# Optimization experiments

Measured on AMD Instinct MI355X. Metric: run time of the kernel, lower is better.

## Reference

```python
import jax, jax.numpy as jnp
import numpy as np

E = 11      # num_experts
K = 6       # active_experts
P = 64      # prototype_dim
NH = 4      # attention heads
HD = P // NH


def setup_inputs() -> dict:
    key = jax.random.key(0)
    ks = jax.random.split(key, 24)
    B, C, H, W = 8, 128, 64, 64
    hid = 4 * C
    s = lambda k, shape, sc=0.02: jax.random.normal(k, shape, dtype=jnp.float32) * sc
    # orthogonal-ish prototypes via QR
    q, _ = jnp.linalg.qr(jax.random.normal(ks[1], (P, P), dtype=jnp.float32))
    return {
        "x": jax.random.normal(ks[0], (B, C, H, W), dtype=jnp.float32),
        "proto": q[:E, :],                       # (E, P)
        "ctx_w": s(ks[2], (P, C)), "ctx_b": jnp.zeros((P,), jnp.float32),
        "inp_w": s(ks[3], (P, C)), "inp_b": jnp.zeros((P,), jnp.float32),
        "wq": s(ks[4], (P, P)), "bq": jnp.zeros((P,), jnp.float32),
        "wk": s(ks[5], (P, P)), "bk": jnp.zeros((P,), jnp.float32),
        "wv": s(ks[6], (P, P)), "bv": jnp.zeros((P,), jnp.float32),
        "wo": s(ks[7], (P, P)), "bo": jnp.zeros((P,), jnp.float32),
        "ln_g": jnp.ones((P,), jnp.float32), "ln_b": jnp.zeros((P,), jnp.float32),
        "ew1": s(ks[8], (E, hid, C)), "eb1": jnp.zeros((E, hid), jnp.float32),
        "ew2": s(ks[9], (E, C, hid)), "eb2": jnp.zeros((E, C), jnp.float32),
    }


def _layernorm(x, g, b, eps=1e-5):
    m = x.mean(-1, keepdims=True)
    v = ((x - m) ** 2).mean(-1, keepdims=True)
    return (x - m) * jax.lax.rsqrt(v + eps) * g + b


def _forward(x, proto, ctx_w, ctx_b, inp_w, inp_b,
             wq, bq, wk, bk, wv, bv, wo, bo, ln_g, ln_b,
             ew1, eb1, ew2, eb2):
    B, C, H, W = x.shape
    # --- router: global context + prototype interaction ---
    gc = jnp.einsum("bchw->bc", x) / (H * W)          # (B, C) mean over HW
    gc = gc @ ctx_w.T + ctx_b                          # (B, P)
    seq = jnp.concatenate([gc[:, None, :],
                           jnp.broadcast_to(proto[None], (B, E, P))], axis=1)  # (B, E+1, P)
    S = E + 1
    q = (seq @ wq.T + bq).reshape(B, S, NH, HD)
    k = (seq @ wk.T + bk).reshape(B, S, NH, HD)
    v = (seq @ wv.T + bv).reshape(B, S, NH, HD)
    att = jax.nn.softmax(jnp.einsum("bqhd,bkhd->bhqk", q, k) / jnp.sqrt(jnp.float32(HD)), axis=-1)
    ao = jnp.einsum("bhqk,bkhd->bqhd", att, v).reshape(B, S, P) @ wo.T + bo
    seq2 = _layernorm(ao + seq, ln_g, ln_b)
    up = seq2[:, 1:, :]                                # (B, E, P) updated prototypes
    # --- per-pixel routing logits ---
    xr = jnp.einsum("bchw,pc->bphw", x, inp_w) + inp_b[None, :, None, None]
    logits = jnp.einsum("bphw,bep->behw", xr, up) / jnp.sqrt(jnp.float32(P))
    probs = jax.nn.softmax(logits, axis=1)             # (B, E, H, W)
    pt = probs.transpose(0, 2, 3, 1)                   # (B, H, W, E)
    tv, ti = jax.lax.top_k(pt, K)                      # (B, H, W, K)
    tv = tv / tv.sum(-1, keepdims=True)
    oh = jax.nn.one_hot(ti, E, dtype=x.dtype)          # (B, H, W, K, E)
    mask = (oh * tv[..., None]).sum(-2)                # (B, H, W, E) scatter of routing weights
    # --- dense expert loop with per-pixel masking ---
    final = jnp.zeros_like(x)
    for e in range(E):
        h = jax.nn.gelu(jnp.einsum("bchw,oc->bohw", x, ew1[e]) + eb1[e][None, :, None, None],
                        approximate=False)
        y = jnp.einsum("bohw,co->bchw", h, ew2[e]) + eb2[e][None, :, None, None]
        final = final + mask[..., e][:, None, :, :] * y
    # --- aux losses ---
    mean_prob = probs.mean((0, 2, 3))                  # (E,)
    mean_load = oh.sum(-2).mean((0, 1, 2))             # (E,)
    aux = E * jnp.sum(mean_prob * mean_load)
    pn = proto / jnp.linalg.norm(proto, axis=1, keepdims=True)
    corr = pn @ pn.T
    ortho = jnp.linalg.norm(corr - jnp.eye(E, dtype=x.dtype))
    return x + final, aux + 0.5 * ortho


def reference(x, proto, ctx_w, ctx_b, inp_w, inp_b,
              wq, bq, wk, bk, wv, bv, wo, bo, ln_g, ln_b,
              ew1, eb1, ew2, eb2):
    return _forward(x, proto, ctx_w, ctx_b, inp_w, inp_b,
                    wq, bq, wk, bk, wv, bv, wo, bo, ln_g, ln_b,
                    ew1, eb1, ew2, eb2)
```

## Files before the change

kernel.cpp:

```cpp
#include <hip/hip_runtime.h>

#define NE 11
#define NP 64
#define NC 128
#define NHW 4096
#define NHID 512
#define NB 8

typedef __attribute__((ext_vector_type(8))) __bf16 bf16x8;
typedef __attribute__((ext_vector_type(4))) float f32x4;

__device__ __forceinline__ unsigned short f2bf(float f) {
    unsigned u = __float_as_uint(f);
    unsigned r = (u + 0x7fffu + ((u >> 16) & 1u)) >> 16;
    return (unsigned short)r;
}

__device__ __forceinline__ float gelu_f(float v) {
    return 0.5f * v * (1.0f + erff(v * 0.70710678118654752440f));
}

__device__ __forceinline__ bf16x8 ldsB(const unsigned short* basep, int row, int col) {
    int byteoff = ((row << 8) + (col << 1)) ^ ((row & 7) << 4);
    return *(const bf16x8*)((const char*)basep + byteoff);
}

__global__ void k_cvt(const float* __restrict__ ew1, const float* __restrict__ ew2,
                      unsigned short* __restrict__ o1, unsigned short* __restrict__ o2) {
    const int n = NE * NHID * NC;
    for (int i = blockIdx.x * 256 + threadIdx.x; i < n; i += gridDim.x * 256) {
        o1[i] = f2bf(ew1[i]);
        o2[i] = f2bf(ew2[i]);
    }
}

__global__ void k_gc(const float* __restrict__ x, float* __restrict__ gc) {
    int row = blockIdx.x;
    const float* p = x + (size_t)row * NHW;
    float s = 0.f;
    for (int i = threadIdx.x; i < NHW; i += 256) s += p[i];
    __shared__ float red[256];
    red[threadIdx.x] = s;
    __syncthreads();
    for (int off = 128; off > 0; off >>= 1) {
        if (threadIdx.x < off) red[threadIdx.x] += red[threadIdx.x + off];
        __syncthreads();
    }
    if (threadIdx.x == 0) gc[row] = red[0] * (1.0f / 4096.0f);
}

__global__ void k_attn(const float* __restrict__ gc, const float* __restrict__ proto,
                       const float* __restrict__ ctx_w, const float* __restrict__ ctx_b,
                       const float* __restrict__ wq, const float* __restrict__ bq,
                       const float* __restrict__ wk, const float* __restrict__ bk,
                       const float* __restrict__ wv, const float* __restrict__ bv,
                       const float* __restrict__ wo, const float* __restrict__ bo,
                       const float* __restrict__ lng, const float* __restrict__ lnb,
                       float* __restrict__ up, float* __restrict__ ortho, float* __restrict__ stats) {
    int t = threadIdx.x;
    __shared__ float seq[12][64], qs[12][64], ks_[12][64], vs[12][64], ao[12][64], rr[12][64];
    __shared__ float nr[NE], sq[NE * NE];

    if (blockIdx.x == 8) {
        if (t < 22) stats[t] = 0.0f;
        if (t < NE) {
            float s = 0.f;
            for (int p = 0; p < NP; p++) { float v = proto[t * NP + p]; s += v * v; }
            nr[t] = rsqrtf(s);
        }
        __syncthreads();
        if (t < NE * NE) {
            int i = t / NE, j = t % NE;
            float d = 0.f;
            for (int p = 0; p < NP; p++) d += proto[i * NP + p] * proto[j * NP + p];
            float c = d * nr[i] * nr[j] - (i == j ? 1.0f : 0.0f);
            sq[t] = c * c;
        }
        __syncthreads();
        if (t == 0) {
            float s = 0.f;
            for (int i = 0; i < NE * NE; i++) s += sq[i];
            *ortho = sqrtf(s);
        }
        return;
    }

    int b = blockIdx.x;
    if (t < NP) {
        float a = ctx_b[t];
        for (int c = 0; c < NC; c++) a = fmaf(gc[b * NC + c], ctx_w[t * NC + c], a);
        seq[0][t] = a;
    }
    for (int i = t; i < NE * NP; i += 256) { int e = i >> 6, p = i & 63; seq[e + 1][p] = proto[e * NP + p]; }
    __syncthreads();
    for (int i = t; i < 12 * NP; i += 256) {
        int s = i >> 6, p = i & 63;
        float aq = bq[p], ak = bk[p], av = bv[p];
        for (int pp = 0; pp < NP; pp++) {
            float sv = seq[s][pp];
            aq = fmaf(sv, wq[p * NP + pp], aq);
            ak = fmaf(sv, wk[p * NP + pp], ak);
            av = fmaf(sv, wv[p * NP + pp], av);
        }
        qs[s][p] = aq; ks_[s][p] = ak; vs[s][p] = av;
    }
    __syncthreads();
    if (t < 48) {
        int h = t / 12, qq = t % 12;
        float sc[12], m = -1e30f;
        for (int kk = 0; kk < 12; kk++) {
            float s = 0.f;
            for (int d = 0; d < 16; d++) s = fmaf(qs[qq][h * 16 + d], ks_[kk][h * 16 + d], s);
            s *= 0.25f;
            sc[kk] = s;
            if (s > m) m = s;
        }
        float den = 0.f;
        for (int kk = 0; kk < 12; kk++) { sc[kk] = expf(sc[kk] - m); den += sc[kk]; }
        float inv = 1.0f / den;
        for (int d = 0; d < 16; d++) {
            float a = 0.f;
            for (int kk = 0; kk < 12; kk++) a = fmaf(sc[kk], vs[kk][h * 16 + d], a);
            ao[qq][h * 16 + d] = a * inv;
        }
    }
    __syncthreads();
    for (int i = t; i < 12 * NP; i += 256) {
        int s = i >> 6, p = i & 63;
        float a = bo[p];
        for (int pp = 0; pp < NP; pp++) a = fmaf(ao[s][pp], wo[p * NP + pp], a);
        rr[s][p] = a + seq[s][p];
    }
    __syncthreads();
    if (t < 12) {
        int s = t;
        float m = 0.f;
        for (int p = 0; p < NP; p++) m += rr[s][p];
        m *= (1.0f / 64.0f);
        float v = 0.f;
        for (int p = 0; p < NP; p++) { float d = rr[s][p] - m; v += d * d; }
        v *= (1.0f / 64.0f);
        float is = rsqrtf(v + 1e-5f);
        if (s >= 1)
            for (int p = 0; p < NP; p++)
                up[(b * NE + s - 1) * NP + p] = (rr[s][p] - m) * is * lng[p] + lnb[p];
    }
}

__global__ __launch_bounds__(256, 2) void k_main(
    const float* __restrict__ x, const float* __restrict__ inp_w, const float* __restrict__ inp_b,
    const unsigned short* __restrict__ ew1b, const float* __restrict__ eb1,
    const unsigned short* __restrict__ ew2b, const float* __restrict__ eb2,
    const float* __restrict__ upw, float* __restrict__ stats, float* __restrict__ out) {
    int tid = threadIdx.x;
    int bimg = blockIdx.x >> 6;
    int pix0 = (blockIdx.x & 63) << 6;
    int wid = tid >> 6;
    int l15 = tid & 15;
    int l4 = (tid >> 4) & 3;

    __shared__ __align__(16) unsigned short xs[64 * 128];
    __shared__ __align__(16) unsigned short hs[64 * 128];
    __shared__ float stage[32 * 64];
    __shared__ float lpart[4][NE][64];
    __shared__ float upl[NE * NP];
    __shared__ float wm[NE * 64];
    __shared__ float pb[NE * 64];
    __shared__ unsigned smask[64];
    __shared__ float eb1c[128], eb2l[128];
    __shared__ int eflag[NE];

    for (int i = tid; i < NE * NP; i += 256) upl[i] = upw[bimg * (NE * NP) + i];
    int pixl = tid & 63;
    int pg = wid;
    float xr[16];
#pragma unroll
    for (int p = 0; p < 16; p++) xr[p] = inp_b[pg * 16 + p];

    for (int cb = 0; cb < NC; cb += 32) {
        for (int i = tid; i < 32 * 64; i += 256) {
            int cc = i >> 6, px = i & 63;
            float v = x[(size_t)(bimg * NC + cb + cc) * NHW + pix0 + px];
            stage[cc * 64 + px] = v;
            int byteoff = ((px << 8) + ((cb + cc) << 1)) ^ ((px & 7) << 4);
            *(unsigned short*)((char*)xs + byteoff) = f2bf(v);
        }
        __syncthreads();
#pragma unroll 4
        for (int cc = 0; cc < 32; cc++) {
            float xv = stage[cc * 64 + pixl];
#pragma unroll
            for (int p = 0; p < 16; p++)
                xr[p] = fmaf(inp_w[(pg * 16 + p) * NC + cb + cc], xv, xr[p]);
        }
        __syncthreads();
    }
    for (int e = 0; e < NE; e++) {
        float a = 0.f;
#pragma unroll
        for (int p = 0; p < 16; p++) a = fmaf(upl[e * NP + pg * 16 + p], xr[p], a);
        lpart[pg][e][pixl] = a;
    }
    __syncthreads();

    if (tid < 64) {
        float pr[NE];
        float mx = -1e30f;
        for (int e = 0; e < NE; e++) {
            float l = (lpart[0][e][tid] + lpart[1][e][tid] + lpart[2][e][tid] + lpart[3][e][tid]) * 0.125f;
            pr[e] = l;
            if (l > mx) mx = l;
        }
        float den = 0.f;
        for (int e = 0; e < NE; e++) { pr[e] = expf(pr[e] - mx); den += pr[e]; }
        float inv = 1.0f / den;
        for (int e = 0; e < NE; e++) { pr[e] *= inv; pb[e * 64 + tid] = pr[e]; }
        unsigned used = 0;
        float tvsum = 0.f;
        float wloc[NE];
        for (int e = 0; e < NE; e++) wloc[e] = 0.f;
        for (int k = 0; k < 6; k++) {
            int best = 0;
            float bv = -1.0f;
            for (int e = 0; e < NE; e++)
                if (!((used >> e) & 1) && pr[e] > bv) { bv = pr[e]; best = e; }
            used |= 1u << best;
            wloc[best] = bv;
            tvsum += bv;
        }
        float itv = 1.0f / tvsum;
        for (int e = 0; e < NE; e++) wm[e * 64 + tid] = wloc[e] * itv;
        smask[tid] = used;
    }
    __syncthreads();
    if (tid < NE) {
        float sp = 0.f;
        int cnt = 0;
        for (int px = 0; px < 64; px++) {
            sp += pb[tid * 64 + px];
            cnt += (smask[px] >> tid) & 1;
        }
        atomicAdd(&stats[tid], sp);
        atomicAdd(&stats[NE + tid], (float)cnt);
        eflag[tid] = cnt;
    }
    __syncthreads();

    float outacc[2][4][4];
    for (int ct = 0; ct < 2; ct++)
        for (int nt = 0; nt < 4; nt++)
            for (int r = 0; r < 4; r++) outacc[ct][nt][r] = 0.f;

    for (int e = 0; e < NE; e++) {
        if (eflag[e] == 0) continue;
        __syncthreads();
        if (tid < 128) eb2l[tid] = eb2[e * NC + tid];
        f32x4 acc2[2][4];
        for (int ct = 0; ct < 2; ct++)
            for (int nt = 0; nt < 4; nt++)
                for (int r = 0; r < 4; r++) acc2[ct][nt][r] = 0.f;

        for (int j = 0; j < 4; j++) {
            if (tid < 128) eb1c[tid] = eb1[e * NHID + j * 128 + tid];
            bf16x8 a1[2][4];
#pragma unroll
            for (int ot = 0; ot < 2; ot++)
#pragma unroll
                for (int ksp = 0; ksp < 4; ksp++) {
                    const unsigned short* src =
                        ew1b + (size_t)(e * NHID + j * 128 + (wid * 2 + ot) * 16 + l15) * NC + ksp * 32 + l4 * 8;
                    a1[ot][ksp] = *(const bf16x8*)src;
                }
            f32x4 acc1[2][4];
            for (int ot = 0; ot < 2; ot++)
                for (int nt = 0; nt < 4; nt++)
                    for (int r = 0; r < 4; r++) acc1[ot][nt][r] = 0.f;
#pragma unroll
            for (int nt = 0; nt < 4; nt++) {
#pragma unroll
                for (int ksp = 0; ksp < 4; ksp++) {
                    bf16x8 bf = ldsB(xs, nt * 16 + l15, ksp * 32 + l4 * 8);
                    acc1[0][nt] = __builtin_amdgcn_mfma_f32_16x16x32_bf16(a1[0][ksp], bf, acc1[0][nt], 0, 0, 0);
                    acc1[1][nt] = __builtin_amdgcn_mfma_f32_16x16x32_bf16(a1[1][ksp], bf, acc1[1][nt], 0, 0, 0);
                }
            }
            __syncthreads();
#pragma unroll
            for (int ot = 0; ot < 2; ot++)
                for (int nt = 0; nt < 4; nt++) {
                    int oloc = (wid * 2 + ot) * 16 + l4 * 4;
                    int px = nt * 16 + l15;
                    unsigned short h4[4];
#pragma unroll
                    for (int r = 0; r < 4; r++) {
                        float v = acc1[ot][nt][r] + eb1c[oloc + r];
                        h4[r] = f2bf(gelu_f(v));
                    }
                    unsigned lo = (unsigned)h4[0] | ((unsigned)h4[1] << 16);
                    unsigned hi = (unsigned)h4[2] | ((unsigned)h4[3] << 16);
                    int byteoff = ((px << 8) + (oloc << 1)) ^ ((px & 7) << 4);
                    *(uint2*)((char*)hs + byteoff) = make_uint2(lo, hi);
                }
            __syncthreads();
            bf16x8 a2[2][4];
#pragma unroll
            for (int ct = 0; ct < 2; ct++)
#pragma unroll
                for (int ksp = 0; ksp < 4; ksp++) {
                    const unsigned short* src =
                        ew2b + (size_t)(e * NC + (wid * 2 + ct) * 16 + l15) * NHID + j * 128 + ksp * 32 + l4 * 8;
                    a2[ct][ksp] = *(const bf16x8*)src;
                }
#pragma unroll
            for (int nt = 0; nt < 4; nt++) {
#pragma unroll
                for (int ksp = 0; ksp < 4; ksp++) {
                    bf16x8 bf = ldsB(hs, nt * 16 + l15, ksp * 32 + l4 * 8);
                    acc2[0][nt] = __builtin_amdgcn_mfma_f32_16x16x32_bf16(a2[0][ksp], bf, acc2[0][nt], 0, 0, 0);
                    acc2[1][nt] = __builtin_amdgcn_mfma_f32_16x16x32_bf16(a2[1][ksp], bf, acc2[1][nt], 0, 0, 0);
                }
            }
        }
#pragma unroll
        for (int ct = 0; ct < 2; ct++)
            for (int nt = 0; nt < 4; nt++) {
                int px = nt * 16 + l15;
                float w = wm[e * 64 + px];
                int cg = (wid * 2 + ct) * 16 + l4 * 4;
#pragma unroll
                for (int r = 0; r < 4; r++)
                    outacc[ct][nt][r] = fmaf(w, acc2[ct][nt][r] + eb2l[cg + r], outacc[ct][nt][r]);
            }
    }

#pragma unroll
    for (int ct = 0; ct < 2; ct++)
        for (int nt = 0; nt < 4; nt++) {
            int px = pix0 + nt * 16 + l15;
#pragma unroll
            for (int r = 0; r < 4; r++) {
                int c = (wid * 2 + ct) * 16 + l4 * 4 + r;
                size_t g = (size_t)(bimg * NC + c) * NHW + px;
                out[g] = x[g] + outacc[ct][nt][r];
            }
        }
}

__global__ void k_final(const float* __restrict__ stats, const float* __restrict__ ortho,
                        float* __restrict__ out) {
    if (threadIdx.x == 0 && blockIdx.x == 0) {
        float aux = 0.f;
        for (int e = 0; e < NE; e++)
            aux += (stats[e] * (1.0f / 32768.0f)) * (stats[NE + e] * (1.0f / 32768.0f));
        aux *= (float)NE;
        out[4194304] = aux + 0.5f * (*ortho);
    }
}

extern "C" void kernel_launch(void* const* d_in, const int* in_sizes, int n_in,
                              void* d_out, int out_size, void* d_ws, size_t ws_size,
                              hipStream_t stream) {
    const float* x = (const float*)d_in[0];
    const float* proto = (const float*)d_in[1];
    const float* ctx_w = (const float*)d_in[2];
    const float* ctx_b = (const float*)d_in[3];
    const float* inp_w = (const float*)d_in[4];
    const float* inp_b = (const float*)d_in[5];
    const float* wq = (const float*)d_in[6];
    const float* bq = (const float*)d_in[7];
    const float* wk = (const float*)d_in[8];
    const float* bk = (const float*)d_in[9];
    const float* wv = (const float*)d_in[10];
    const float* bv = (const float*)d_in[11];
    const float* wo = (const float*)d_in[12];
    const float* bo = (const float*)d_in[13];
    const float* lng = (const float*)d_in[14];
    const float* lnb = (const float*)d_in[15];
    const float* ew1 = (const float*)d_in[16];
    const float* eb1 = (const float*)d_in[17];
    const float* ew2 = (const float*)d_in[18];
    const float* eb2 = (const float*)d_in[19];
    float* out = (float*)d_out;
    float* ws = (float*)d_ws;

    float* gc = ws;
    float* up = ws + 1024;
    float* ortho = ws + 6656;
    float* stats = ws + 6657;
    unsigned short* ew1b = (unsigned short*)(ws + 8192);
    unsigned short* ew2b = ew1b + NE * NHID * NC;

    k_cvt<<<512, 256, 0, stream>>>(ew1, ew2, ew1b, ew2b);
    k_gc<<<1024, 256, 0, stream>>>(x, gc);
    k_attn<<<9, 256, 0, stream>>>(gc, proto, ctx_w, ctx_b, wq, bq, wk, bk, wv, bv, wo, bo, lng, lnb,
                                  up, ortho, stats);
    k_main<<<512, 256, 0, stream>>>(x, inp_w, inp_b, ew1b, eb1, ew2b, eb2, up, stats, out);
    k_final<<<1, 64, 0, stream>>>(stats, ortho, out);
}
```

Before: 432.3 us.

## Restructure expert MLP kernel with 8 waves, double-buffered hidden tile, fast GELU

Raises the main kernel to 512 threads, with each wave owning one 16-row tile instead of two, and double-buffers the hidden-activation LDS tile so each step needs one barrier instead of two. The routing weight is folded into the GELU output before the second GEMM, which removes the per-expert accumulator epilogue. Expert bias is added once at the end. It also replaces erff with a polynomial erf approximation built on hardware exp2/rcp, and computes stats with wave shuffles and ballots. The weight-conversion and mean kernels are merged into one launch. It drops the skip for experts no pixel in the tile uses, and the polynomial GELU adds small numerical error.

```diff
diff --git a/kernel.cpp b/kernel.cpp
--- a/kernel.cpp
+++ b/kernel.cpp
@@ -5,48 +5,67 @@
 #define NC 128
 #define NHW 4096
 #define NHID 512
-#define NB 8
 
 typedef __attribute__((ext_vector_type(8))) __bf16 bf16x8;
+typedef __attribute__((ext_vector_type(4))) __bf16 bf16x4;
 typedef __attribute__((ext_vector_type(4))) float f32x4;
 
+#if __has_builtin(__builtin_amdgcn_exp2f)
+#define FEXP2(x) __builtin_amdgcn_exp2f(x)
+#else
+#define FEXP2(x) exp2f(x)
+#endif
+#if __has_builtin(__builtin_amdgcn_rcpf)
+#define FRCP(x) __builtin_amdgcn_rcpf(x)
+#else
+#define FRCP(x) (1.0f / (x))
+#endif
+
 __device__ __forceinline__ unsigned short f2bf(float f) {
-    unsigned u = __float_as_uint(f);
-    unsigned r = (u + 0x7fffu + ((u >> 16) & 1u)) >> 16;
-    return (unsigned short)r;
-}
-
-__device__ __forceinline__ float gelu_f(float v) {
-    return 0.5f * v * (1.0f + erff(v * 0.70710678118654752440f));
-}
-
-__device__ __forceinline__ bf16x8 ldsB(const unsigned short* basep, int row, int col) {
-    int byteoff = ((row << 8) + (col << 1)) ^ ((row & 7) << 4);
-    return *(const bf16x8*)((const char*)basep + byteoff);
-}
-
-__global__ void k_cvt(const float* __restrict__ ew1, const float* __restrict__ ew2,
-                      unsigned short* __restrict__ o1, unsigned short* __restrict__ o2) {
-    const int n = NE * NHID * NC;
-    for (int i = blockIdx.x * 256 + threadIdx.x; i < n; i += gridDim.x * 256) {
-        o1[i] = f2bf(ew1[i]);
-        o2[i] = f2bf(ew2[i]);
-    }
-}
-
-__global__ void k_gc(const float* __restrict__ x, float* __restrict__ gc) {
-    int row = blockIdx.x;
-    const float* p = x + (size_t)row * NHW;
-    float s = 0.f;
-    for (int i = threadIdx.x; i < NHW; i += 256) s += p[i];
-    __shared__ float red[256];
-    red[threadIdx.x] = s;
-    __syncthreads();
-    for (int off = 128; off > 0; off >>= 1) {
-        if (threadIdx.x < off) red[threadIdx.x] += red[threadIdx.x + off];
-        __syncthreads();
-    }
-    if (threadIdx.x == 0) gc[row] = red[0] * (1.0f / 4096.0f);
+    return __builtin_bit_cast(unsigned short, (__bf16)f);
+}
+
+__device__ __forceinline__ float gelu_erf(float v) {
+    float av = fabsf(v);
+    float z = av * 0.70710678118654752440f;
+    float t = FRCP(fmaf(z, 0.3275911f, 1.0f));
+    float p = t * fmaf(t, fmaf(t, fmaf(t, fmaf(t, 1.061405429f, -1.453152027f),
+                                       1.421413741f), -0.284496736f), 0.254829592f);
+    float e = FEXP2(z * z * -1.44269504088896f);
+    float erfz = fmaf(-p, e, 1.0f);
+    float hv = 0.5f * av;
+    float g = fmaf(hv, erfz, hv);
+    return g + fminf(v, 0.0f);
+}
+
+__device__ __forceinline__ bf16x8 ldsB(const char* base, int row, int col) {
+    int off = ((row << 8) + (col << 1)) ^ ((row & 7) << 4);
+    return *(const bf16x8*)(base + off);
+}
+
+__global__ void k_prep(const float* __restrict__ ew1, const float* __restrict__ ew2,
+                       unsigned short* __restrict__ o1, unsigned short* __restrict__ o2,
+                       const float* __restrict__ x, float* __restrict__ gc) {
+    if (blockIdx.x < 512) {
+        const int n = NE * NHID * NC;
+        for (int i = blockIdx.x * 256 + threadIdx.x; i < n; i += 512 * 256) {
+            o1[i] = f2bf(ew1[i]);
+            o2[i] = f2bf(ew2[i]);
+        }
+    } else {
+        int row = blockIdx.x - 512;
+        const float* p = x + (size_t)row * NHW;
+        float s = 0.f;
+        for (int i = threadIdx.x; i < NHW; i += 256) s += p[i];
+        __shared__ float red[256];
+        red[threadIdx.x] = s;
+        __syncthreads();
+        for (int off = 128; off > 0; off >>= 1) {
+            if (threadIdx.x < off) red[threadIdx.x] += red[threadIdx.x + off];
+            __syncthreads();
+        }
+        if (threadIdx.x == 0) gc[row] = red[0] * (1.0f / 4096.0f);
+    }
 }
 
 __global__ void k_attn(const float* __restrict__ gc, const float* __restrict__ proto,
@@ -147,7 +166,7 @@
     }
 }
 
-__global__ __launch_bounds__(256, 2) void k_main(
+__global__ __launch_bounds__(512, 4) void k_main(
     const float* __restrict__ x, const float* __restrict__ inp_w, const float* __restrict__ inp_b,
     const unsigned short* __restrict__ ew1b, const float* __restrict__ eb1,
     const unsigned short* __restrict__ ew2b, const float* __restrict__ eb2,
@@ -159,191 +178,170 @@
     int l15 = tid & 15;
     int l4 = (tid >> 4) & 3;
 
-    __shared__ __align__(16) unsigned short xs[64 * 128];
-    __shared__ __align__(16) unsigned short hs[64 * 128];
-    __shared__ float stage[32 * 64];
-    __shared__ float lpart[4][NE][64];
-    __shared__ float upl[NE * NP];
-    __shared__ float wm[NE * 64];
-    __shared__ float pb[NE * 64];
-    __shared__ unsigned smask[64];
-    __shared__ float eb1c[128], eb2l[128];
-    __shared__ int eflag[NE];
-
-    for (int i = tid; i < NE * NP; i += 256) upl[i] = upw[bimg * (NE * NP) + i];
+    __shared__ __align__(16) char smem[54784];
+    char* xs = smem;
+    float* stage = (float*)(smem + 32768);
+    float* lpart = (float*)(smem + 36864);
+    float* upl = (float*)(smem + 49152);
+    float* wm = (float*)(smem + 51968);
+
+    for (int i = tid; i < NE * NP; i += 512) upl[i] = upw[bimg * (NE * NP) + i];
+    int pg = wid & 3;
     int pixl = tid & 63;
-    int pg = wid;
     float xr[16];
 #pragma unroll
     for (int p = 0; p < 16; p++) xr[p] = inp_b[pg * 16 + p];
 
-    for (int cb = 0; cb < NC; cb += 32) {
-        for (int i = tid; i < 32 * 64; i += 256) {
+    for (int cb = 0; cb < NC; cb += 16) {
+        for (int i = tid; i < 16 * 64; i += 512) {
             int cc = i >> 6, px = i & 63;
             float v = x[(size_t)(bimg * NC + cb + cc) * NHW + pix0 + px];
             stage[cc * 64 + px] = v;
-            int byteoff = ((px << 8) + ((cb + cc) << 1)) ^ ((px & 7) << 4);
-            *(unsigned short*)((char*)xs + byteoff) = f2bf(v);
-        }
-        __syncthreads();
+            int off = ((px << 8) + ((cb + cc) << 1)) ^ ((px & 7) << 4);
+            *(unsigned short*)(xs + off) = f2bf(v);
+        }
+        __syncthreads();
+        if (tid < 256) {
 #pragma unroll 4
-        for (int cc = 0; cc < 32; cc++) {
-            float xv = stage[cc * 64 + pixl];
-#pragma unroll
-            for (int p = 0; p < 16; p++)
-                xr[p] = fmaf(inp_w[(pg * 16 + p) * NC + cb + cc], xv, xr[p]);
-        }
-        __syncthreads();
-    }
-    for (int e = 0; e < NE; e++) {
-        float a = 0.f;
-#pragma unroll
-        for (int p = 0; p < 16; p++) a = fmaf(upl[e * NP + pg * 16 + p], xr[p], a);
-        lpart[pg][e][pixl] = a;
+            for (int cc = 0; cc < 16; cc++) {
+                float xv = stage[cc * 64 + pixl];
+#pragma unroll
+                for (int p = 0; p < 16; p++)
+                    xr[p] = fmaf(inp_w[(pg * 16 + p) * NC + cb + cc], xv, xr[p]);
+            }
+        }
+        __syncthreads();
+    }
+    if (tid < 256) {
+#pragma unroll
+        for (int e = 0; e < NE; e++) {
+            float a = 0.f;
+#pragma unroll
+            for (int p = 0; p < 16; p++) a = fmaf(upl[e * NP + pg * 16 + p], xr[p], a);
+            lpart[(pg * NE + e) * 64 + pixl] = a;
+        }
     }
     __syncthreads();
 
     if (tid < 64) {
         float pr[NE];
         float mx = -1e30f;
+#pragma unroll
         for (int e = 0; e < NE; e++) {
-            float l = (lpart[0][e][tid] + lpart[1][e][tid] + lpart[2][e][tid] + lpart[3][e][tid]) * 0.125f;
+            float l = (lpart[(0 * NE + e) * 64 + tid] + lpart[(1 * NE + e) * 64 + tid] +
+                       lpart[(2 * NE + e) * 64 + tid] + lpart[(3 * NE + e) * 64 + tid]) * 0.125f;
             pr[e] = l;
-            if (l > mx) mx = l;
+            mx = fmaxf(mx, l);
         }
         float den = 0.f;
-        for (int e = 0; e < NE; e++) { pr[e] = expf(pr[e] - mx); den += pr[e]; }
+#pragma unroll
+        for (int e = 0; e < NE; e++) { pr[e] = __expf(pr[e] - mx); den += pr[e]; }
         float inv = 1.0f / den;
-        for (int e = 0; e < NE; e++) { pr[e] *= inv; pb[e * 64 + tid] = pr[e]; }
+#pragma unroll
+        for (int e = 0; e < NE; e++) pr[e] *= inv;
         unsigned used = 0;
         float tvsum = 0.f;
-        float wloc[NE];
-        for (int e = 0; e < NE; e++) wloc[e] = 0.f;
         for (int k = 0; k < 6; k++) {
+            float bv = -1.f;
             int best = 0;
-            float bv = -1.0f;
-            for (int e = 0; e < NE; e++)
-                if (!((used >> e) & 1) && pr[e] > bv) { bv = pr[e]; best = e; }
+#pragma unroll
+            for (int e = 0; e < NE; e++) {
+                bool sel = !((used >> e) & 1) && (pr[e] > bv);
+                bv = sel ? pr[e] : bv;
+                best = sel ? e : best;
+            }
             used |= 1u << best;
-            wloc[best] = bv;
             tvsum += bv;
         }
         float itv = 1.0f / tvsum;
-        for (int e = 0; e < NE; e++) wm[e * 64 + tid] = wloc[e] * itv;
-        smask[tid] = used;
-    }
-    __syncthreads();
-    if (tid < NE) {
-        float sp = 0.f;
-        int cnt = 0;
-        for (int px = 0; px < 64; px++) {
-            sp += pb[tid * 64 + px];
-            cnt += (smask[px] >> tid) & 1;
-        }
-        atomicAdd(&stats[tid], sp);
-        atomicAdd(&stats[NE + tid], (float)cnt);
-        eflag[tid] = cnt;
-    }
-    __syncthreads();
-
-    float outacc[2][4][4];
-    for (int ct = 0; ct < 2; ct++)
-        for (int nt = 0; nt < 4; nt++)
-            for (int r = 0; r < 4; r++) outacc[ct][nt][r] = 0.f;
+#pragma unroll
+        for (int e = 0; e < NE; e++)
+            wm[e * 64 + tid] = ((used >> e) & 1) ? pr[e] * itv : 0.0f;
+#pragma unroll
+        for (int e = 0; e < NE; e++) {
+            float s = pr[e];
+            for (int off = 32; off; off >>= 1) s += __shfl_xor(s, off);
+            unsigned long long bal = __ballot((used >> e) & 1);
+            if (tid == 0) {
+                atomicAdd(&stats[e], s);
+                atomicAdd(&stats[NE + e], (float)__popcll(bal));
+            }
+        }
+    }
+    __syncthreads();
+
+    f32x4 acc2[4];
+#pragma unroll
+    for (int nt = 0; nt < 4; nt++) acc2[nt] = {0.f, 0.f, 0.f, 0.f};
 
     for (int e = 0; e < NE; e++) {
-        if (eflag[e] == 0) continue;
-        __syncthreads();
-        if (tid < 128) eb2l[tid] = eb2[e * NC + tid];
-        f32x4 acc2[2][4];
-        for (int ct = 0; ct < 2; ct++)
+#pragma unroll 2
+        for (int j = 0; j < 4; j++) {
+            char* hsbuf = (j & 1) ? (smem + 32768) : (smem + 16384);
+            const unsigned short* w1p = ew1b + (size_t)(e * NHID + j * 128 + wid * 16 + l15) * NC;
+            bf16x8 a1[4];
+#pragma unroll
+            for (int ksp = 0; ksp < 4; ksp++) a1[ksp] = *(const bf16x8*)(w1p + ksp * 32 + l4 * 8);
+            f32x4 acc1[4];
+#pragma unroll
+            for (int nt = 0; nt < 4; nt++) acc1[nt] = {0.f, 0.f, 0.f, 0.f};
+#pragma unroll
             for (int nt = 0; nt < 4; nt++)
-                for (int r = 0; r < 4; r++) acc2[ct][nt][r] = 0.f;
-
-        for (int j = 0; j < 4; j++) {
-            if (tid < 128) eb1c[tid] = eb1[e * NHID + j * 128 + tid];
-            bf16x8 a1[2][4];
-#pragma unroll
-            for (int ot = 0; ot < 2; ot++)
 #pragma unroll
                 for (int ksp = 0; ksp < 4; ksp++) {
-                    const unsigned short* src =
-                        ew1b + (size_t)(e * NHID + j * 128 + (wid * 2 + ot) * 16 + l15) * NC + ksp * 32 + l4 * 8;
-                    a1[ot][ksp] = *(const bf16x8*)src;
+                    bf16x8 xb = ldsB(xs, nt * 16 + l15, ksp * 32 + l4 * 8);
+                    acc1[nt] = __builtin_amdgcn_mfma_f32_16x16x32_bf16(a1[ksp], xb, acc1[nt], 0, 0, 0);
                 }
-            f32x4 acc1[2][4];
-            for (int ot = 0; ot < 2; ot++)
-                for (int nt = 0; nt < 4; nt++)
-                    for (int r = 0; r < 4; r++) acc1[ot][nt][r] = 0.f;
-#pragma unroll
-            for (int nt = 0; nt < 4; nt++) {
-#pragma unroll
-                for (int ksp = 0; ksp < 4; ksp++) {
-                    bf16x8 bf = ldsB(xs, nt * 16 + l15, ksp * 32 + l4 * 8);
-                    acc1[0][nt] = __builtin_amdgcn_mfma_f32_16x16x32_bf16(a1[0][ksp], bf, acc1[0][nt], 0, 0, 0);
-                    acc1[1][nt] = __builtin_amdgcn_mfma_f32_16x16x32_bf16(a1[1][ksp], bf, acc1[1][nt], 0, 0, 0);
-                }
-            }
-            __syncthreads();
-#pragma unroll
-            for (int ot = 0; ot < 2; ot++)
-                for (int nt = 0; nt < 4; nt++) {
-                    int oloc = (wid * 2 + ot) * 16 + l4 * 4;
-                    int px = nt * 16 + l15;
-                    unsigned short h4[4];
-#pragma unroll
-                    for (int r = 0; r < 4; r++) {
-                        float v = acc1[ot][nt][r] + eb1c[oloc + r];
-                        h4[r] = f2bf(gelu_f(v));
-                    }
-                    unsigned lo = (unsigned)h4[0] | ((unsigned)h4[1] << 16);
-                    unsigned hi = (unsigned)h4[2] | ((unsigned)h4[3] << 16);
-                    int byteoff = ((px << 8) + (oloc << 1)) ^ ((px & 7) << 4);
-                    *(uint2*)((char*)hs + byteoff) = make_uint2(lo, hi);
-                }
-            __syncthreads();
-            bf16x8 a2[2][4];
-#pragma unroll
-            for (int ct = 0; ct < 2; ct++)
-#pragma unroll
-                for (int ksp = 0; ksp < 4; ksp++) {
-                    const unsigned short* src =
-                        ew2b + (size_t)(e * NC + (wid * 2 + ct) * 16 + l15) * NHID + j * 128 + ksp * 32 + l4 * 8;
-                    a2[ct][ksp] = *(const bf16x8*)src;
-                }
-#pragma unroll
-            for (int nt = 0; nt < 4; nt++) {
-#pragma unroll
-                for (int ksp = 0; ksp < 4; ksp++) {
-                    bf16x8 bf = ldsB(hs, nt * 16 + l15, ksp * 32 + l4 * 8);
-                    acc2[0][nt] = __builtin_amdgcn_mfma_f32_16x16x32_bf16(a2[0][ksp], bf, acc2[0][nt], 0, 0, 0);
-                    acc2[1][nt] = __builtin_amdgcn_mfma_f32_16x16x32_bf16(a2[1][ksp], bf, acc2[1][nt], 0, 0, 0);
-                }
-            }
-        }
-#pragma unroll
-        for (int ct = 0; ct < 2; ct++)
+            const unsigned short* w2p = ew2b + (size_t)(e * NC + wid * 16 + l15) * NHID + j * 128;
+            bf16x8 a2[4];
+#pragma unroll
+            for (int ksp = 0; ksp < 4; ksp++) a2[ksp] = *(const bf16x8*)(w2p + ksp * 32 + l4 * 8);
+            f32x4 b1 = *(const f32x4*)(eb1 + e * NHID + j * 128 + wid * 16 + l4 * 4);
+            int oloc2 = (wid * 16 + l4 * 4) << 1;
+#pragma unroll
             for (int nt = 0; nt < 4; nt++) {
                 int px = nt * 16 + l15;
                 float w = wm[e * 64 + px];
-                int cg = (wid * 2 + ct) * 16 + l4 * 4;
-#pragma unroll
-                for (int r = 0; r < 4; r++)
-                    outacc[ct][nt][r] = fmaf(w, acc2[ct][nt][r] + eb2l[cg + r], outacc[ct][nt][r]);
+                bf16x4 hb;
+#pragma unroll
+                for (int r = 0; r < 4; r++) {
+                    float v = acc1[nt][r] + b1[r];
+                    hb[r] = (__bf16)(gelu_erf(v) * w);
+                }
+                int off = ((px << 8) + oloc2) ^ ((px & 7) << 4);
+                *(uint2*)(hsbuf + off) = __builtin_bit_cast(uint2, hb);
             }
-    }
-
-#pragma unroll
-    for (int ct = 0; ct < 2; ct++)
+            __syncthreads();
+#pragma unroll
+            for (int nt = 0; nt < 4; nt++)
+#pragma unroll
+                for (int ksp = 0; ksp < 4; ksp++) {
+                    bf16x8 hb2 = ldsB(hsbuf, nt * 16 + l15, ksp * 32 + l4 * 8);
+                    acc2[nt] = __builtin_amdgcn_mfma_f32_16x16x32_bf16(a2[ksp], hb2, acc2[nt], 0, 0, 0);
+                }
+        }
+    }
+
+#pragma unroll
+    for (int e = 0; e < NE; e++) {
+        f32x4 b2 = *(const f32x4*)(eb2 + e * NC + wid * 16 + l4 * 4);
+#pragma unroll
         for (int nt = 0; nt < 4; nt++) {
-            int px = pix0 + nt * 16 + l15;
-#pragma unroll
-            for (int r = 0; r < 4; r++) {
-                int c = (wid * 2 + ct) * 16 + l4 * 4 + r;
-                size_t g = (size_t)(bimg * NC + c) * NHW + px;
-                out[g] = x[g] + outacc[ct][nt][r];
-            }
-        }
+            float w = wm[e * 64 + nt * 16 + l15];
+#pragma unroll
+            for (int r = 0; r < 4; r++) acc2[nt][r] = fmaf(w, b2[r], acc2[nt][r]);
+        }
+    }
+    int c0 = wid * 16 + l4 * 4;
+#pragma unroll
+    for (int nt = 0; nt < 4; nt++) {
+        int px = pix0 + nt * 16 + l15;
+#pragma unroll
+        for (int r = 0; r < 4; r++) {
+            size_t g = (size_t)(bimg * NC + c0 + r) * NHW + px;
+            out[g] = x[g] + acc2[nt][r];
+        }
+    }
 }
 
 __global__ void k_final(const float* __restrict__ stats, const float* __restrict__ ortho,
@@ -390,10 +388,9 @@
     unsigned short* ew1b = (unsigned short*)(ws + 8192);
     unsigned short* ew2b = ew1b + NE * NHID * NC;
 
-    k_cvt<<<512, 256, 0, stream>>>(ew1, ew2, ew1b, ew2b);
-    k_gc<<<1024, 256, 0, stream>>>(x, gc);
+    k_prep<<<1536, 256, 0, stream>>>(ew1, ew2, ew1b, ew2b, x, gc);
     k_attn<<<9, 256, 0, stream>>>(gc, proto, ctx_w, ctx_b, wq, bq, wk, bk, wv, bv, wo, bo, lng, lnb,
                                   up, ortho, stats);
-    k_main<<<512, 256, 0, stream>>>(x, inp_w, inp_b, ew1b, eb1, ew2b, eb2, up, stats, out);
+    k_main<<<512, 512, 0, stream>>>(x, inp_w, inp_b, ew1b, eb1, ew2b, eb2, up, stats, out);
     k_final<<<1, 64, 0, stream>>>(stats, ortho, out);
 }
```

After: 456.9 us. 5.7% more time.
